# Optimization experiments

Measured on AMD Instinct MI355X. Metric: run time of the kernel, lower is better.

The kernel has to match this reference:

```python
import jax, jax.numpy as jnp
import numpy as np

D_MODEL = 1024
MAX_LEN = 2048
BATCH = 4


def _causal_mask(max_len):
    # tril ones -> 0 on/below diag, -inf above (added to scores BEFORE scaling,
    # matching the original module's order of operations)
    return jnp.where(jnp.tril(jnp.ones((max_len, max_len), dtype=bool)), 0.0, -jnp.inf).astype(jnp.float32)


def setup_inputs() -> dict:
    key = jax.random.key(0)
    ks = jax.random.split(key, 9)
    s = 1.0 / np.sqrt(D_MODEL)  # torch Linear default init scale (uniform bound)
    return {
        "encoded_q": jax.random.normal(ks[0], (BATCH, MAX_LEN, D_MODEL), jnp.float32),
        "encoded_k": jax.random.normal(ks[1], (BATCH, MAX_LEN, D_MODEL), jnp.float32),
        "encoded_v": jax.random.normal(ks[2], (BATCH, MAX_LEN, D_MODEL), jnp.float32),
        "W_q": jax.random.uniform(ks[3], (D_MODEL, D_MODEL), jnp.float32, -s, s),
        "b_q": jax.random.uniform(ks[4], (D_MODEL,), jnp.float32, -s, s),
        "W_k": jax.random.uniform(ks[5], (D_MODEL, D_MODEL), jnp.float32, -s, s),
        "b_k": jax.random.uniform(ks[6], (D_MODEL,), jnp.float32, -s, s),
        "W_v": jax.random.uniform(ks[7], (D_MODEL, D_MODEL), jnp.float32, -s, s),
        "b_v": jax.random.uniform(ks[8], (D_MODEL,), jnp.float32, -s, s),
        "parameter_mask": 1,
    }


def reference(encoded_q, encoded_k, encoded_v, W_q, b_q, W_k, b_k, W_v, b_v, parameter_mask):
    # torch Linear: y = x @ W.T + b
    q = jnp.einsum("bsd,ed->bse", encoded_q, W_q) + b_q  # [B,S,D]
    k = jnp.einsum("bsd,ed->bse", encoded_k, W_k) + b_k
    v = jnp.einsum("bsd,ed->bse", encoded_v, W_v) + b_v
    values = jnp.einsum("bqd,bkd->bqk", q, k)  # [B,S,S]
    if parameter_mask:
        values = values + _causal_mask(values.shape[-1])
    scaled = values / jnp.sqrt(jnp.float32(D_MODEL))
    attn = jax.nn.softmax(scaled, axis=-1)
    return jnp.einsum("bqk,bkd->bqd", attn, v)  # [B,S,D]
```

## Files before the change

### kernel.cpp

```cpp
#include <hip/hip_runtime.h>

typedef __bf16 bf16;
typedef __attribute__((ext_vector_type(8))) __bf16 bf16x8;
typedef __attribute__((ext_vector_type(4))) __bf16 bf16x4;
typedef __attribute__((ext_vector_type(4))) float f32x4;

#define S_LEN 2048
#define DM 1024
#define NB 4

__device__ __forceinline__ void async_copy16(const void* g, void* l)
{
    __builtin_amdgcn_global_load_lds(
        (const __attribute__((address_space(1))) unsigned int*)g,
        (__attribute__((address_space(3))) unsigned int*)l,
        16, 0, 0);
}

#define VM_WAIT8 asm volatile("s_waitcnt vmcnt(8)" ::: "memory")
#define VM_WAIT0 asm volatile("s_waitcnt vmcnt(0)" ::: "memory")
#define LGKM0    asm volatile("s_waitcnt lgkmcnt(0)" ::: "memory")
#define BAR      asm volatile("s_barrier" ::: "memory")


__device__ __forceinline__ void stage_issue(const char* aGk, size_t aRow32,
                                            const char* bGk, size_t bRow32,
                                            char* aL, char* bL)
{
#pragma unroll
    for (int i = 0; i < 4; i++) {
        async_copy16(aGk + i * aRow32, aL + i * 4096);
        async_copy16(bGk + i * bRow32, bL + i * 4096);
    }
}

__device__ __forceinline__ void read_frags(const char* bufA, const char* bufB,
                                           int wr, int wc, int l16, int quad,
                                           bf16x8 (&af)[2][4], bf16x8 (&bfr)[2][4])
{
    const int swz = l16 & 7;
#pragma unroll
    for (int kk = 0; kk < 2; kk++) {
        const int col = (((kk << 2) + quad) ^ swz) << 4;
#pragma unroll
        for (int t = 0; t < 4; t++) {
            af[kk][t]  = *(const bf16x8*)(bufA + (wr * 64 + t * 16 + l16) * 128 + col);
            bfr[kk][t] = *(const bf16x8*)(bufB + (wc * 64 + t * 16 + l16) * 128 + col);
        }
    }
}

__device__ __forceinline__ void mfma_all(const bf16x8 (&af)[2][4],
                                         const bf16x8 (&bfr)[2][4],
                                         f32x4 (&acc)[4][4])
{
#pragma unroll
    for (int kk = 0; kk < 2; kk++)
#pragma unroll
        for (int rt = 0; rt < 4; rt++)
#pragma unroll
            for (int ct = 0; ct < 4; ct++)
                acc[rt][ct] = __builtin_amdgcn_mfma_f32_16x16x32_bf16(
                    af[kk][rt], bfr[kk][ct], acc[rt][ct], 0, 0, 0);
}

__device__ __forceinline__ void gemm_tile(
    const bf16* __restrict__ A, int lda,
    const bf16* __restrict__ B, int ldb,
    int kSteps, char* smem, f32x4 (&acc)[4][4])
{
    const int tid = threadIdx.x;
    const int w = tid >> 6, lane = tid & 63;
    const int quad = lane >> 4, l16 = lane & 15;
    const int wr = w >> 1, wc = w & 1;

#pragma unroll
    for (int i = 0; i < 4; i++)
#pragma unroll
        for (int j = 0; j < 4; j++) acc[i][j] = f32x4{0.f, 0.f, 0.f, 0.f};

    const int srow = tid >> 3;
    const int sc8  = tid & 7;
    const int srcCol = (sc8 ^ (srow & 7)) * 16;
    const char* aG = (const char*)(A + (size_t)srow * lda) + srcCol;
    const char* bG = (const char*)(B + (size_t)srow * ldb) + srcCol;
    const size_t aRow32 = (size_t)lda * 64;
    const size_t bRow32 = (size_t)ldb * 64;
    char* aL0 = smem +     0 + w * 1024;
    char* bL0 = smem + 16384 + w * 1024;
    char* aL1 = smem + 32768 + w * 1024;
    char* bL1 = smem + 49152 + w * 1024;

    stage_issue(aG,       aRow32, bG,       bRow32, aL0, bL0);
    stage_issue(aG + 128, aRow32, bG + 128, bRow32, aL1, bL1);

    for (int ks = 0; ks < kSteps; ks += 2) {
        const bool more = (ks + 2 < kSteps);
        bf16x8 af[2][4], bfr[2][4];

        VM_WAIT8;
        BAR;
        read_frags(smem, smem + 16384, wr, wc, l16, quad, af, bfr);
        LGKM0;
        BAR;
        if (more)
            stage_issue(aG + (size_t)(ks + 2) * 128, aRow32,
                        bG + (size_t)(ks + 2) * 128, bRow32, aL0, bL0);
        mfma_all(af, bfr, acc);

        if (more) { VM_WAIT8; } else { VM_WAIT0; }
        BAR;
        read_frags(smem + 32768, smem + 49152, wr, wc, l16, quad, af, bfr);
        LGKM0;
        BAR;
        if (more)
            stage_issue(aG + (size_t)(ks + 3) * 128, aRow32,
                        bG + (size_t)(ks + 3) * 128, bRow32, aL1, bL1);
        mfma_all(af, bfr, acc);
    }
}

__global__ __launch_bounds__(256) void prep_kernel(
    const float* __restrict__ Wq, const float* __restrict__ Wk, const float* __restrict__ Wv,
    const float* __restrict__ Eq, const float* __restrict__ Ek, const float* __restrict__ Ev,
    bf16* __restrict__ Wqb, bf16* __restrict__ Wkb, bf16* __restrict__ Wvb,
    bf16* __restrict__ Eqb, bf16* __restrict__ Ekb, bf16* __restrict__ Evb,
    float* __restrict__ lsum)
{
    const int bid = blockIdx.x;
    const int tid = threadIdx.x;
    if (bid == 0) {
        for (int j = tid; j < NB * S_LEN; j += 256) lsum[j] = 0.0f;
        return;
    }
    const float* src;
    bf16* dst;
    size_t i;
    if (bid <= 1536) {
        const int q = bid - 1;
        const int z = q >> 9;
        src = z == 0 ? Wq : z == 1 ? Wk : Wv;
        dst = z == 0 ? Wqb : z == 1 ? Wkb : Wvb;
        i = ((size_t)(q & 511) * 256 + tid) * 8;
    } else {
        const int q = bid - 1537;
        const int z = q >> 12;
        src = z == 0 ? Eq : z == 1 ? Ek : Ev;
        dst = z == 0 ? Eqb : z == 1 ? Ekb : Evb;
        i = ((size_t)(q & 4095) * 256 + tid) * 8;
    }
    f32x4 a = *(const f32x4*)(src + i);
    f32x4 b = *(const f32x4*)(src + i + 4);
    bf16x8 o;
    o[0] = (bf16)a[0]; o[1] = (bf16)a[1]; o[2] = (bf16)a[2]; o[3] = (bf16)a[3];
    o[4] = (bf16)b[0]; o[5] = (bf16)b[1]; o[6] = (bf16)b[2]; o[7] = (bf16)b[3];
    *(bf16x8*)(dst + i) = o;
}

__global__ __launch_bounds__(256) void projqk_kernel(
    const bf16* __restrict__ Eq, const bf16* __restrict__ Ek,
    const bf16* __restrict__ Wq, const bf16* __restrict__ Wk,
    const float* __restrict__ bq, const float* __restrict__ bk,
    bf16* __restrict__ Qo, bf16* __restrict__ Ko)
{
    __shared__ __align__(16) char smem[65536];
    const int bid = blockIdx.x;
    const int c = bid & 7;
    const int j = bid >> 3;
    const int z = j >> 6;
    const int r64 = j & 63;
    const int m0 = (c * 8 + (r64 >> 3)) * 128;
    const int n0 = (r64 & 7) * 128;

    const bf16* E     = z == 0 ? Eq : Ek;
    const bf16* W     = z == 0 ? Wq : Wk;
    const float* bias = z == 0 ? bq : bk;

    f32x4 acc[4][4];
    gemm_tile(E + (size_t)m0 * DM, DM, W + (size_t)n0 * DM, DM, DM / 64, smem, acc);

    const int tid = threadIdx.x;
    const int w = tid >> 6, lane = tid & 63;
    const int quad = lane >> 4, l16 = lane & 15;
    const int wr = w >> 1, wc = w & 1;
    const int nBase = n0 + wc * 64;

    float bcol[4];
#pragma unroll
    for (int ct = 0; ct < 4; ct++) bcol[ct] = bias[nBase + ct * 16 + l16];

    __syncthreads();
    bf16* Tt = (bf16*)smem;
#pragma unroll
    for (int rt = 0; rt < 4; rt++)
#pragma unroll
        for (int ct = 0; ct < 4; ct++)
#pragma unroll
            for (int r = 0; r < 4; r++)
                Tt[(wr * 64 + rt * 16 + quad * 4 + r) * 136 + wc * 64 + ct * 16 + l16]
                    = (bf16)(acc[rt][ct][r] + bcol[ct]);
    __syncthreads();
    bf16* O = z == 0 ? Qo : Ko;
    const int row = tid >> 1, half = tid & 1;
    const bf16* src = Tt + row * 136 + half * 64;
    bf16* dst = O + (size_t)(m0 + row) * DM + n0 + half * 64;
#pragma unroll
    for (int i = 0; i < 8; i++)
        *(bf16x8*)(dst + i * 8) = *(const bf16x8*)(src + i * 8);
}

__global__ __launch_bounds__(256) void projv_qk_kernel(
    const bf16* __restrict__ Ev, const bf16* __restrict__ Wv,
    const float* __restrict__ bv, bf16* __restrict__ Vt,
    const bf16* __restrict__ Q, const bf16* __restrict__ K,
    const int* __restrict__ maskp, bf16* __restrict__ P, float* __restrict__ lsum)
{
    __shared__ __align__(16) char smem[65536];
    const int bid = blockIdx.x;
    const int tid = threadIdx.x;
    const int w = tid >> 6, lane = tid & 63;
    const int quad = lane >> 4, l16 = lane & 15;
    const int wr = w >> 1, wc = w & 1;

    if (bid < 512) {
        const int c = bid & 7;
        const int r64 = bid >> 3;
        const int m0 = (c * 8 + (r64 >> 3)) * 128;
        const int n0 = (r64 & 7) * 128;

        f32x4 acc[4][4];
        gemm_tile(Ev + (size_t)m0 * DM, DM, Wv + (size_t)n0 * DM, DM, DM / 64, smem, acc);

        const int nBase = n0 + wc * 64;
        float bcol[4];
#pragma unroll
        for (int ct = 0; ct < 4; ct++) bcol[ct] = bv[nBase + ct * 16 + l16];

        const int mBase = m0 + wr * 64;
#pragma unroll
        for (int rt = 0; rt < 4; rt++) {
            const int m = mBase + rt * 16 + quad * 4;
            const int bb = m >> 11;
            const int s  = m & 2047;
#pragma unroll
            for (int ct = 0; ct < 4; ct++) {
                const int n = nBase + ct * 16 + l16;
                bf16x4 o;
                o[0] = (bf16)(acc[rt][ct][0] + bcol[ct]);
                o[1] = (bf16)(acc[rt][ct][1] + bcol[ct]);
                o[2] = (bf16)(acc[rt][ct][2] + bcol[ct]);
                o[3] = (bf16)(acc[rt][ct][3] + bcol[ct]);
                *(bf16x4*)(Vt + ((size_t)(bb * DM + n)) * S_LEN + s) = o;
            }
        }
    } else {
        const int qbid = bid - 512;
        const int c = qbid & 7;
        const int j = qbid >> 3;
        const int b = j >> 5;
        const int jj = j & 31;
        const int kt = (jj < 16) ? c : (15 - c);
        const int qt = jj & 15;
        const bool causal = (maskp[0] != 0);
        if (causal && kt > qt) return;

        f32x4 acc[4][4];
        const bf16* Qb = Q + ((size_t)(b * S_LEN + qt * 128)) * DM;
        const bf16* Kb = K + ((size_t)(b * S_LEN + kt * 128)) * DM;
        gemm_tile(Qb, DM, Kb, DM, DM / 64, smem, acc);

        const float scale = 0.03125f;

        __syncthreads();
        bf16* Pt = (bf16*)smem;
#pragma unroll
        for (int rt = 0; rt < 4; rt++)
#pragma unroll
            for (int r = 0; r < 4; r++) {
                const int rloc = wr * 64 + rt * 16 + quad * 4 + r;
                const int qg = qt * 128 + rloc;
#pragma unroll
                for (int ct = 0; ct < 4; ct++) {
                    const int kg = kt * 128 + wc * 64 + ct * 16 + l16;
                    float p = (!causal || kg <= qg) ? __expf(acc[rt][ct][r] * scale) : 0.0f;
                    Pt[rloc * 136 + wc * 64 + ct * 16 + l16] = (bf16)p;
                }
            }
        __syncthreads();

        bf16* Pb = P + (size_t)b * S_LEN * S_LEN;
        float* lb = lsum + b * S_LEN;
        const int row = tid >> 1, half = tid & 1;
        const bf16* src = Pt + row * 136 + half * 64;
        bf16* dst = Pb + (size_t)(qt * 128 + row) * S_LEN + kt * 128 + half * 64;
        float rs = 0.0f;
#pragma unroll
        for (int i = 0; i < 8; i++) {
            bf16x8 x = *(const bf16x8*)(src + i * 8);
            *(bf16x8*)(dst + i * 8) = x;
#pragma unroll
            for (int e = 0; e < 8; e++) rs += (float)x[e];
        }
        rs += __shfl_xor(rs, 1);
        if (half == 0) atomicAdd(&lb[qt * 128 + row], rs);
    }
}

__global__ __launch_bounds__(256) void pv_kernel(
    const bf16* __restrict__ P, const bf16* __restrict__ Vt,
    const float* __restrict__ lsum, const int* __restrict__ maskp,
    float* __restrict__ Out)
{
    const int bid = blockIdx.x;
    const int c = bid & 7;
    const int b = c >> 1;
    const int par = c & 1;
    const int idx = bid >> 3;
    const int dt = idx & 7;
    const int qi = idx >> 3;
    const int kk = (qi + dt) & 7;
    const unsigned tbl = par ? 0x695A2D1Eu : 0x784B3C0Fu;
    const int qt = (tbl >> (kk * 4)) & 15;
    const bool causal = (maskp[0] != 0);
    const int kSteps = causal ? (qt + 1) * 2 : (S_LEN / 64);

    __shared__ __align__(16) char smem[65536];

    f32x4 acc[4][4];
    const bf16* Pb = P + ((size_t)b * S_LEN + qt * 128) * S_LEN;
    const bf16* Vb = Vt + ((size_t)(b * DM + dt * 128)) * S_LEN;
    gemm_tile(Pb, S_LEN, Vb, S_LEN, kSteps, smem, acc);

    const int tid = threadIdx.x;
    const int w = tid >> 6, lane = tid & 63;
    const int quad = lane >> 4, l16 = lane & 15;
    const int wr = w >> 1, wc = w & 1;

    const float* lb = lsum + b * S_LEN;
    float inv[4][4];
#pragma unroll
    for (int rt = 0; rt < 4; rt++)
#pragma unroll
        for (int r = 0; r < 4; r++)
            inv[rt][r] = 1.0f / lb[qt * 128 + wr * 64 + rt * 16 + quad * 4 + r];

    __syncthreads();
    float* Ot = (float*)smem;
#pragma unroll
    for (int h = 0; h < 2; h++) {
        if (wr == h) {
#pragma unroll
            for (int rt = 0; rt < 4; rt++)
#pragma unroll
                for (int r = 0; r < 4; r++) {
                    const int rloc = rt * 16 + quad * 4 + r;
#pragma unroll
                    for (int ct = 0; ct < 4; ct++)
                        Ot[rloc * 132 + wc * 64 + ct * 16 + l16] = acc[rt][ct][r] * inv[rt][r];
                }
        }
        __syncthreads();
        const int row = tid >> 2, qq = tid & 3;
        const float* src = Ot + row * 132 + qq * 32;
        float* dst = Out + (size_t)(b * S_LEN + qt * 128 + h * 64 + row) * DM + dt * 128 + qq * 32;
#pragma unroll
        for (int i = 0; i < 8; i++)
            *(f32x4*)(dst + i * 4) = *(const f32x4*)(src + i * 4);
        __syncthreads();
    }
}

extern "C" void kernel_launch(void* const* d_in, const int* in_sizes, int n_in,
                              void* d_out, int out_size, void* d_ws, size_t ws_size,
                              hipStream_t stream)
{
    const float* Eq = (const float*)d_in[0];
    const float* Ek = (const float*)d_in[1];
    const float* Ev = (const float*)d_in[2];
    const float* Wq = (const float*)d_in[3];
    const float* bq = (const float*)d_in[4];
    const float* Wk = (const float*)d_in[5];
    const float* bk = (const float*)d_in[6];
    const float* Wv = (const float*)d_in[7];
    const float* bv = (const float*)d_in[8];
    const int* maskp = (const int*)d_in[9];
    float* Out = (float*)d_out;

    char* ws = (char*)d_ws;
    const size_t SZ_QKV = (size_t)NB * S_LEN * DM * 2;
    const size_t SZ_W   = (size_t)DM * DM * 2;
    bf16* Qb  = (bf16*)(ws);
    bf16* Kb  = (bf16*)(ws + SZ_QKV);
    bf16* Vtb = (bf16*)(ws + 2 * SZ_QKV);
    bf16* Wqb = (bf16*)(ws + 3 * SZ_QKV);
    bf16* Wkb = (bf16*)(ws + 3 * SZ_QKV + SZ_W);
    bf16* Wvb = (bf16*)(ws + 3 * SZ_QKV + 2 * SZ_W);
    float* lsum = (float*)(ws + 3 * SZ_QKV + 3 * SZ_W);
    bf16* Pbuf = (bf16*)(ws + 3 * SZ_QKV + 3 * SZ_W + (1 << 20));
    bf16* Eqb = Pbuf;
    bf16* Ekb = Eqb + (size_t)NB * S_LEN * DM;
    bf16* Evb = Ekb + (size_t)NB * S_LEN * DM;

    prep_kernel<<<13825, 256, 0, stream>>>(
        Wq, Wk, Wv, Eq, Ek, Ev, Wqb, Wkb, Wvb, Eqb, Ekb, Evb, lsum);

    projqk_kernel<<<1024, 256, 0, stream>>>(
        Eqb, Ekb, Wqb, Wkb, bq, bk, Qb, Kb);

    projv_qk_kernel<<<1536, 256, 0, stream>>>(
        Evb, Wvb, bv, Vtb, Qb, Kb, maskp, Pbuf, lsum);

    pv_kernel<<<512, 256, 0, stream>>>(Pbuf, Vtb, lsum, maskp, Out);
}
```

Measured before the change: 289.5 us.

## Split heavy causal PV tiles along K with atomic accumulation into zeroed output

The PV kernel now launches 1024 blocks. The heavy query tiles (upper half, long causal K ranges) are split into two K-chunks whose partial results are atomically added into Out. Light tiles are computed whole and stored directly. The prep kernel zeroes the Out rows that receive atomics. This is meant to even out the per-block work imbalance from causal masking and fill more CUs, at the cost of extra zeroing traffic, float atomics and nondeterministic summation order.

```diff
diff --git a/kernel.cpp b/kernel.cpp
--- a/kernel.cpp
+++ b/kernel.cpp
@@ -125,7 +125,7 @@
     const float* __restrict__ Eq, const float* __restrict__ Ek, const float* __restrict__ Ev,
     bf16* __restrict__ Wqb, bf16* __restrict__ Wkb, bf16* __restrict__ Wvb,
     bf16* __restrict__ Eqb, bf16* __restrict__ Ekb, bf16* __restrict__ Evb,
-    float* __restrict__ lsum)
+    float* __restrict__ lsum, float* __restrict__ Out, const int* __restrict__ maskp)
 {
     const int bid = blockIdx.x;
     const int tid = threadIdx.x;
@@ -133,17 +133,29 @@
         for (int j = tid; j < NB * S_LEN; j += 256) lsum[j] = 0.0f;
         return;
     }
+    if (bid <= 2048) {
+        const int z = bid - 1;
+        const size_t o = (size_t)z * 16384;
+        const int rowInBatch = (int)((o >> 12) & (S_LEN - 1));
+        const bool causal = (maskp[0] != 0);
+        if (causal && rowInBatch < 1024) return;
+        f32x4* p = (f32x4*)((char*)Out + o);
+        const f32x4 zv = {0.f, 0.f, 0.f, 0.f};
+#pragma unroll
+        for (int i = 0; i < 4; i++) p[tid + 256 * i] = zv;
+        return;
+    }
     const float* src;
     bf16* dst;
     size_t i;
-    if (bid <= 1536) {
-        const int q = bid - 1;
+    if (bid <= 3584) {
+        const int q = bid - 2049;
         const int z = q >> 9;
         src = z == 0 ? Wq : z == 1 ? Wk : Wv;
         dst = z == 0 ? Wqb : z == 1 ? Wkb : Wvb;
         i = ((size_t)(q & 511) * 256 + tid) * 8;
     } else {
-        const int q = bid - 1537;
+        const int q = bid - 3585;
         const int z = q >> 12;
         src = z == 0 ? Eq : z == 1 ? Ek : Ev;
         dst = z == 0 ? Eqb : z == 1 ? Ekb : Evb;
@@ -312,24 +324,36 @@
     float* __restrict__ Out)
 {
     const int bid = blockIdx.x;
-    const int c = bid & 7;
+    const bool heavy = bid < 512;
+    const int v = heavy ? bid : bid - 512;
+    const int c = v & 7;
     const int b = c >> 1;
     const int par = c & 1;
-    const int idx = bid >> 3;
-    const int dt = idx & 7;
-    const int qi = idx >> 3;
-    const int kk = (qi + dt) & 7;
-    const unsigned tbl = par ? 0x695A2D1Eu : 0x784B3C0Fu;
-    const int qt = (tbl >> (kk * 4)) & 15;
+    const int u = v >> 3;
+    const int dt = u & 7;
+    const int ch = (u >> 5) & 1;
+    const int qti = 3 - ((u >> 3) & 3);
+    const int qt = heavy ? (8 + qti * 2 + par) : (qti * 2 + par);
     const bool causal = (maskp[0] != 0);
-    const int kSteps = causal ? (qt + 1) * 2 : (S_LEN / 64);
+    const int kTotal = causal ? (qt + 1) * 2 : (S_LEN / 64);
+
+    const bool whole = causal && !heavy;
+    int sBeg, sCnt;
+    if (whole) {
+        if (ch == 1) return;
+        sBeg = 0; sCnt = kTotal;
+    } else {
+        const int s0 = ((kTotal / 2) + 1) & ~1;
+        if (ch == 0) { sBeg = 0;  sCnt = s0; }
+        else         { sBeg = s0; sCnt = kTotal - s0; if (sCnt <= 0) return; }
+    }
 
     __shared__ __align__(16) char smem[65536];
 
     f32x4 acc[4][4];
-    const bf16* Pb = P + ((size_t)b * S_LEN + qt * 128) * S_LEN;
-    const bf16* Vb = Vt + ((size_t)(b * DM + dt * 128)) * S_LEN;
-    gemm_tile(Pb, S_LEN, Vb, S_LEN, kSteps, smem, acc);
+    const bf16* Pb = P + ((size_t)b * S_LEN + qt * 128) * S_LEN + (size_t)sBeg * 64;
+    const bf16* Vb = Vt + ((size_t)(b * DM + dt * 128)) * S_LEN + (size_t)sBeg * 64;
+    gemm_tile(Pb, S_LEN, Vb, S_LEN, sCnt, smem, acc);
 
     const int tid = threadIdx.x;
     const int w = tid >> 6, lane = tid & 63;
@@ -344,29 +368,44 @@
         for (int r = 0; r < 4; r++)
             inv[rt][r] = 1.0f / lb[qt * 128 + wr * 64 + rt * 16 + quad * 4 + r];
 
-    __syncthreads();
-    float* Ot = (float*)smem;
-#pragma unroll
-    for (int h = 0; h < 2; h++) {
-        if (wr == h) {
-#pragma unroll
-            for (int rt = 0; rt < 4; rt++)
-#pragma unroll
-                for (int r = 0; r < 4; r++) {
-                    const int rloc = rt * 16 + quad * 4 + r;
-#pragma unroll
-                    for (int ct = 0; ct < 4; ct++)
-                        Ot[rloc * 132 + wc * 64 + ct * 16 + l16] = acc[rt][ct][r] * inv[rt][r];
-                }
+    if (whole) {
+        __syncthreads();
+        float* Ot = (float*)smem;
+#pragma unroll
+        for (int h = 0; h < 2; h++) {
+            if (wr == h) {
+#pragma unroll
+                for (int rt = 0; rt < 4; rt++)
+#pragma unroll
+                    for (int r = 0; r < 4; r++) {
+                        const int rloc = rt * 16 + quad * 4 + r;
+#pragma unroll
+                        for (int ct = 0; ct < 4; ct++)
+                            Ot[rloc * 132 + wc * 64 + ct * 16 + l16] = acc[rt][ct][r] * inv[rt][r];
+                    }
+            }
+            __syncthreads();
+            const int row = tid >> 2, qq = tid & 3;
+            const float* src = Ot + row * 132 + qq * 32;
+            float* dst = Out + (size_t)(b * S_LEN + qt * 128 + h * 64 + row) * DM + dt * 128 + qq * 32;
+#pragma unroll
+            for (int i = 0; i < 8; i++)
+                *(f32x4*)(dst + i * 4) = *(const f32x4*)(src + i * 4);
+            __syncthreads();
         }
-        __syncthreads();
-        const int row = tid >> 2, qq = tid & 3;
-        const float* src = Ot + row * 132 + qq * 32;
-        float* dst = Out + (size_t)(b * S_LEN + qt * 128 + h * 64 + row) * DM + dt * 128 + qq * 32;
-#pragma unroll
-        for (int i = 0; i < 8; i++)
-            *(f32x4*)(dst + i * 4) = *(const f32x4*)(src + i * 4);
-        __syncthreads();
+    } else {
+        const int rowBase = b * S_LEN + qt * 128 + wr * 64;
+        const int colBase = dt * 128 + wc * 64;
+#pragma unroll
+        for (int rt = 0; rt < 4; rt++)
+#pragma unroll
+            for (int r = 0; r < 4; r++) {
+                float* rp = Out + (size_t)(rowBase + rt * 16 + quad * 4 + r) * DM + colBase;
+                const float s = inv[rt][r];
+#pragma unroll
+                for (int ct = 0; ct < 4; ct++)
+                    atomicAdd(rp + ct * 16 + l16, acc[rt][ct][r] * s);
+            }
     }
 }
 
@@ -401,8 +440,8 @@
     bf16* Ekb = Eqb + (size_t)NB * S_LEN * DM;
     bf16* Evb = Ekb + (size_t)NB * S_LEN * DM;
 
-    prep_kernel<<<13825, 256, 0, stream>>>(
-        Wq, Wk, Wv, Eq, Ek, Ev, Wqb, Wkb, Wvb, Eqb, Ekb, Evb, lsum);
+    prep_kernel<<<15873, 256, 0, stream>>>(
+        Wq, Wk, Wv, Eq, Ek, Ev, Wqb, Wkb, Wvb, Eqb, Ekb, Evb, lsum, Out, maskp);
 
     projqk_kernel<<<1024, 256, 0, stream>>>(
         Eqb, Ekb, Wqb, Wkb, bq, bk, Qb, Kb);
@@ -410,5 +449,5 @@
     projv_qk_kernel<<<1536, 256, 0, stream>>>(
         Evb, Wvb, bv, Vtb, Qb, Kb, maskp, Pbuf, lsum);
 
-    pv_kernel<<<512, 256, 0, stream>>>(Pbuf, Vtb, lsum, maskp, Out);
-}
+    pv_kernel<<<1024, 256, 0, stream>>>(Pbuf, Vtb, lsum, maskp, Out);
+}
```

Result: slower. 304.0 us (+5.0%).
